# Kernel optimization log

Hardware: AMD Instinct MI355X
Metric: run time of the kernel (lower is better)

## Reference

```python
import jax, jax.numpy as jnp
import numpy as np


def hadamard_matrix(n):
    # Recursive normalized Hadamard matrix of size 2^n (matches the torch code).
    H = np.array([[1.0]])
    for _ in range(n):
        H = np.block([[H, H], [H, -H]]) / np.sqrt(2.0)
    return jnp.asarray(H, dtype=jnp.float32)


def hadamard_conv(x, filt, bias, H):
    # x: (B, Cin, h, w); filt: (F, kh, kw); bias: (F, 1); H: (n, n)
    n = H.shape[0]
    F, kh, kw = filt.shape
    B, C = x.shape[0], x.shape[1]
    # zero-pad filters and data up to (n, n), then 2D Hadamard transform H A H
    kern = jnp.zeros((F, n, n), x.dtype).at[:, :kh, :kw].set(filt)
    kern_t = jnp.matmul(H, jnp.matmul(kern, H))            # (F, n, n)
    data = jnp.zeros((B, C, n, n), x.dtype).at[:, :, : x.shape[2], : x.shape[3]].set(x)
    data_t = jnp.matmul(H, jnp.matmul(data, H))            # (B, C, n, n)
    # Original: expand to (B, C, F, n, n), multiply by kern_t, inverse transform,
    # then sum over C. Since kern_t is independent of C and the transforms are
    # linear, sum over C first -- identical math, no huge intermediate.
    s = data_t.sum(axis=1)                                  # (B, n, n)
    prod = s[:, None, :, :] * kern_t[None, :, :, :]         # (B, F, n, n)
    out = jnp.matmul(H, jnp.matmul(prod, H))                # (B, F, n, n)
    return out + bias[:, 0][None, :, None, None]


def maxpool2(x):
    # 2x2 max pool, stride 2, on (B, C, H, W)
    return jax.lax.reduce_window(x, -jnp.inf, jax.lax.max, (1, 1, 2, 2), (1, 1, 2, 2), 'VALID')


def setup_inputs() -> dict:
    key = jax.random.key(0)
    ks = jax.random.split(key, 9)
    return {
        'x': jax.random.normal(ks[0], (2048, 3, 32, 32), dtype=jnp.float32),
        'filter1': jax.random.normal(ks[1], (32, 3, 3), dtype=jnp.float32),
        'bias1': jax.random.normal(ks[2], (32, 1), dtype=jnp.float32),
        'filter2': jax.random.normal(ks[3], (64, 3, 3), dtype=jnp.float32),
        'bias2': jax.random.normal(ks[4], (64, 1), dtype=jnp.float32),
        'fc1_w': jax.random.normal(ks[5], (512, 4096), dtype=jnp.float32) * 0.02,
        'fc1_b': jax.random.normal(ks[6], (512,), dtype=jnp.float32) * 0.02,
        'fc2_w': jax.random.normal(ks[7], (10, 512), dtype=jnp.float32) * 0.02,
        'fc2_b': jax.random.normal(ks[8], (10,), dtype=jnp.float32) * 0.02,
    }


def reference(x, filter1, bias1, filter2, bias2, fc1_w, fc1_b, fc2_w, fc2_b):
    H1 = hadamard_matrix(5)  # 32x32
    H2 = hadamard_matrix(4)  # 16x16
    out = hadamard_conv(x, filter1, bias1, H1)      # (B, 32, 32, 32)
    out = maxpool2(jax.nn.relu(out))                # (B, 32, 16, 16)
    out = hadamard_conv(out, filter2, bias2, H2)    # (B, 64, 16, 16)
    out = maxpool2(jax.nn.relu(out))                # (B, 64, 8, 8)
    out = out.reshape(-1, 4096)
    out = jax.nn.relu(out @ fc1_w.T + fc1_b)        # (B, 512)
    out = out @ fc2_w.T + fc2_b                     # (B, 10)
    return jax.nn.softmax(out, axis=1)
```

## Files before the change

### kernel.cpp

```cpp
#include <hip/hip_runtime.h>

#define DEVI __device__ __forceinline__

typedef __attribute__((ext_vector_type(8))) short short8x;
typedef __attribute__((ext_vector_type(4))) float float4x;

DEVI float shx(float v, int m) { return __shfl_xor(v, m, 64); }

DEVI unsigned bf16r(float v) {
  unsigned u = __float_as_uint(v);
  return (u + 0x7FFF + ((u >> 16) & 1)) >> 16;
}
DEVI void split2(float a, float b, unsigned& h, unsigned& l) {
  unsigned ra = bf16r(a), rb = bf16r(b);
  float fa = __uint_as_float(ra << 16), fb = __uint_as_float(rb << 16);
  unsigned la = bf16r(a - fa), lb = bf16r(b - fb);
  h = ra | (rb << 16);
  l = la | (lb << 16);
}

DEVI void gload16(const void* g, void* l) {
  __builtin_amdgcn_global_load_lds(
      (const __attribute__((address_space(1))) void*)g,
      (__attribute__((address_space(3))) void*)l, 16, 0, 0);
}

template <int MASK>
DEVI float lanex(float x) {
  if constexpr (MASK == 1)
    return __int_as_float(__builtin_amdgcn_update_dpp(
        0, __float_as_int(x), 0xB1, 0xF, 0xF, true));
  else if constexpr (MASK == 2)
    return __int_as_float(__builtin_amdgcn_update_dpp(
        0, __float_as_int(x), 0x4E, 0xF, 0xF, true));
  else
    return __int_as_float(__builtin_amdgcn_ds_swizzle(
        __float_as_int(x), (MASK << 10) | 0x1F));
}

__global__ __launch_bounds__(256) void k_conv(
    const float* __restrict__ x, const float* __restrict__ filt1,
    const float* __restrict__ bias1, const float* __restrict__ filt2,
    const float* __restrict__ bias2, unsigned short* __restrict__ Ah,
    unsigned short* __restrict__ Al, const float* __restrict__ fc1w,
    unsigned short* __restrict__ Wh, unsigned short* __restrict__ Wl, int B) {
  __shared__ float sP[4 * 320];
  const int b = blockIdx.x;
  const int tid = threadIdx.x;

  if (b >= B) {
    const int wb = b - B;
#pragma unroll
    for (int q = 0; q < 4; ++q) {
      const int i = wb * 4096 + q * 1024 + tid * 4;
      float4 v = *(const float4*)(fc1w + i);
      unsigned h0, l0, h1, l1;
      split2(v.x, v.y, h0, l0);
      split2(v.z, v.w, h1, l1);
      *(uint2*)(Wh + i) = make_uint2(h0, h1);
      *(uint2*)(Wl + i) = make_uint2(l0, l1);
    }
    return;
  }

  const int wv = tid >> 6, t = tid & 63;

  float s0[16];
  {
    const float* xb = x + (size_t)b * 3072 + (t >> 1) * 32 + (t & 1) * 16;
#pragma unroll
    for (int q = 0; q < 4; ++q) {
      float4 a0 = *(const float4*)(xb + 4 * q);
      float4 a1 = *(const float4*)(xb + 1024 + 4 * q);
      float4 a2 = *(const float4*)(xb + 2048 + 4 * q);
      s0[4 * q + 0] = (a0.x + a1.x + a2.x) * (1.0f / 32.0f);
      s0[4 * q + 1] = (a0.y + a1.y + a2.y) * (1.0f / 32.0f);
      s0[4 * q + 2] = (a0.z + a1.z + a2.z) * (1.0f / 32.0f);
      s0[4 * q + 3] = (a0.w + a1.w + a2.w) * (1.0f / 32.0f);
    }
  }
  float s1[16], s2[16];
#pragma unroll
  for (int k = 0; k < 16; ++k) s1[k] = lanex<2>(s0[k]);
#pragma unroll
  for (int k = 0; k < 16; ++k) s2[k] = lanex<4>(s0[k]);

  float acc[8];
#pragma unroll
  for (int j = 0; j < 8; ++j) acc[j] = 0.0f;

  for (int i = 0; i < 8; ++i) {
    const int f = __builtin_amdgcn_readfirstlane(wv * 8 + i);
    const float* fp = filt1 + f * 9;
    float w[9];
#pragma unroll
    for (int k = 0; k < 9; ++k) w[k] = fp[k];
    const float bb = bias1[f];
    float c[8];
#pragma unroll
    for (int p = 0; p < 8; ++p) {
      const int ja = 2 * p, jb = ja ^ 1;
      const int ja2 = ja ^ 2, jb2 = jb ^ 2;
      float va = fmaf(w[0], s0[ja], bb);
      va = fmaf(w[1], s0[jb], va);
      va = fmaf(w[2], s0[ja2], va);
      va = fmaf(w[3], s1[ja], va);
      va = fmaf(w[4], s1[jb], va);
      va = fmaf(w[5], s1[ja2], va);
      va = fmaf(w[6], s2[ja], va);
      va = fmaf(w[7], s2[jb], va);
      va = fmaf(w[8], s2[ja2], va);
      float vb = fmaf(w[0], s0[jb], bb);
      vb = fmaf(w[1], s0[ja], vb);
      vb = fmaf(w[2], s0[jb2], vb);
      vb = fmaf(w[3], s1[jb], vb);
      vb = fmaf(w[4], s1[ja], vb);
      vb = fmaf(w[5], s1[jb2], vb);
      vb = fmaf(w[6], s2[jb], vb);
      vb = fmaf(w[7], s2[ja], vb);
      vb = fmaf(w[8], s2[jb2], vb);
      c[p] = fmaxf(fmaxf(va, vb), 0.0f);
    }
#pragma unroll
    for (int p = 0; p < 8; ++p) acc[p] += fmaxf(c[p], lanex<2>(c[p]));
  }

  if (!(t & 2)) {
    const int pb = wv * 320 + (t >> 2) * 20 + (t & 1) * 8;
    *(float4*)&sP[pb] = make_float4(acc[0], acc[1], acc[2], acc[3]);
    *(float4*)&sP[pb + 4] = make_float4(acc[4], acc[5], acc[6], acc[7]);
  }
  __syncthreads();

  const int f2s = t >> 4, rr = t & 15;
  float r0[16];
#pragma unroll
  for (int q = 0; q < 4; ++q) {
    float4 s = make_float4(0.f, 0.f, 0.f, 0.f);
#pragma unroll
    for (int w2 = 0; w2 < 4; ++w2) {
      const float4 v = *(const float4*)&sP[w2 * 320 + rr * 20 + 4 * q];
      s.x += v.x; s.y += v.y; s.z += v.z; s.w += v.w;
    }
    r0[4 * q + 0] = s.x * (1.0f / 16.0f);
    r0[4 * q + 1] = s.y * (1.0f / 16.0f);
    r0[4 * q + 2] = s.z * (1.0f / 16.0f);
    r0[4 * q + 3] = s.w * (1.0f / 16.0f);
  }
  float r1[16], r2[16];
#pragma unroll
  for (int k = 0; k < 16; ++k) r1[k] = lanex<1>(r0[k]);
#pragma unroll
  for (int k = 0; k < 16; ++k) r2[k] = lanex<2>(r0[k]);

#pragma unroll
  for (int it = 0; it < 4; ++it) {
    const int g = wv * 16 + it * 4 + f2s;
    const float* gp = filt2 + g * 9;
    float w[9];
#pragma unroll
    for (int k = 0; k < 9; ++k) w[k] = gp[k];
    const float bb = bias2[g];
    float c[8];
#pragma unroll
    for (int p = 0; p < 8; ++p) {
      const int ja = 2 * p, jb = ja ^ 1;
      const int ja2 = ja ^ 2, jb2 = jb ^ 2;
      float va = fmaf(w[0], r0[ja], bb);
      va = fmaf(w[1], r0[jb], va);
      va = fmaf(w[2], r0[ja2], va);
      va = fmaf(w[3], r1[ja], va);
      va = fmaf(w[4], r1[jb], va);
      va = fmaf(w[5], r1[ja2], va);
      va = fmaf(w[6], r2[ja], va);
      va = fmaf(w[7], r2[jb], va);
      va = fmaf(w[8], r2[ja2], va);
      float vb = fmaf(w[0], r0[jb], bb);
      vb = fmaf(w[1], r0[ja], vb);
      vb = fmaf(w[2], r0[jb2], vb);
      vb = fmaf(w[3], r1[jb], vb);
      vb = fmaf(w[4], r1[ja], vb);
      vb = fmaf(w[5], r1[jb2], vb);
      vb = fmaf(w[6], r2[jb], vb);
      vb = fmaf(w[7], r2[ja], vb);
      vb = fmaf(w[8], r2[jb2], vb);
      c[p] = fmaxf(fmaxf(va, vb), 0.0f);
    }
#pragma unroll
    for (int p = 0; p < 8; ++p) c[p] = fmaxf(c[p], lanex<1>(c[p]));
    if (!(t & 1)) {
      unsigned hh[4], ll[4];
#pragma unroll
      for (int j = 0; j < 4; ++j) split2(c[2 * j], c[2 * j + 1], hh[j], ll[j]);
      const size_t off = (size_t)b * 4096 + g * 64 + (rr >> 1) * 8;
      *(uint4*)(Ah + off) = make_uint4(hh[0], hh[1], hh[2], hh[3]);
      *(uint4*)(Al + off) = make_uint4(ll[0], ll[1], ll[2], ll[3]);
    }
  }
}

__global__ __launch_bounds__(256) void k_fc1(
    const unsigned short* __restrict__ Ah, const unsigned short* __restrict__ Al,
    const unsigned short* __restrict__ Wh, const unsigned short* __restrict__ Wl,
    float* __restrict__ P, int M) {
  __shared__ __align__(16) unsigned char lds[49152];
  const int bid = blockIdx.x;
  const int c = bid & 127, nt = bid >> 7;
  const int mt = c >> 2, kidx = c & 3;
  const int m0 = mt * 64, n0 = nt * 64, k0 = kidx * 1024;

  const int tid = threadIdx.x;
  const int wv = tid >> 6, lane = tid & 63;
  const int wm = (wv >> 1) * 32, wn = (wv & 1) * 32;
  const int lm = lane & 15, lq = lane >> 4;
  const int rj = lane >> 3, pj = lane & 7;

  float4x acc[2][2];
#pragma unroll
  for (int i = 0; i < 2; ++i)
#pragma unroll
    for (int j = 0; j < 2; ++j) acc[i][j] = (float4x){0.f, 0.f, 0.f, 0.f};

  auto stage = [&](int st, int bb) {
    const int kcol = k0 + st * 32;
#pragma unroll
    for (int it = 0; it < 2; ++it) {
      const int rb = wv * 16 + it * 8;
      const int r = rb + rj;
      const int l = pj ^ (r & 7);
      const unsigned short* src = (l < 4) ? Ah : Al;
      const size_t go = (size_t)(m0 + r) * 4096 + kcol + (l & 3) * 8;
      gload16(src + go, lds + bb + rb * 128);
    }
#pragma unroll
    for (int it = 0; it < 2; ++it) {
      const int rb = wv * 16 + it * 8;
      const int r = rb + rj;
      const int l = pj ^ (r & 7);
      const unsigned short* src = (l < 4) ? Wh : Wl;
      const size_t go = (size_t)(n0 + r) * 4096 + kcol + (l & 3) * 8;
      gload16(src + go, lds + bb + 8192 + rb * 128);
    }
  };

  stage(0, 0);
  stage(1, 16384);
  asm volatile("s_waitcnt vmcnt(4) lgkmcnt(0)" ::: "memory");
  __builtin_amdgcn_sched_barrier(0);
  __builtin_amdgcn_s_barrier();
  __builtin_amdgcn_sched_barrier(0);

  for (int st = 0; st < 32; ++st) {
    const int bb = (st % 3) * 16384;
    if (st < 30) {
      stage(st + 2, ((st + 2) % 3) * 16384);
      __builtin_amdgcn_sched_barrier(0);
    }

    short8x a_h[2], a_l[2], b_h[2], b_l[2];
#pragma unroll
    for (int fm = 0; fm < 2; ++fm) {
      const int r = wm + fm * 16 + lm;
      const unsigned char* base = lds + bb + r * 128;
      a_h[fm] = *(const short8x*)(base + (lq ^ (r & 7)) * 16);
      a_l[fm] = *(const short8x*)(base + ((lq ^ 4) ^ (r & 7)) * 16);
    }
#pragma unroll
    for (int fn = 0; fn < 2; ++fn) {
      const int r = wn + fn * 16 + lm;
      const unsigned char* base = lds + bb + 8192 + r * 128;
      b_h[fn] = *(const short8x*)(base + (lq ^ (r & 7)) * 16);
      b_l[fn] = *(const short8x*)(base + ((lq ^ 4) ^ (r & 7)) * 16);
    }
#pragma unroll
    for (int fm = 0; fm < 2; ++fm)
#pragma unroll
      for (int fn = 0; fn < 2; ++fn) {
        acc[fm][fn] = __builtin_amdgcn_mfma_f32_16x16x32_bf16(
            a_h[fm], b_h[fn], acc[fm][fn], 0, 0, 0);
        acc[fm][fn] = __builtin_amdgcn_mfma_f32_16x16x32_bf16(
            a_h[fm], b_l[fn], acc[fm][fn], 0, 0, 0);
        acc[fm][fn] = __builtin_amdgcn_mfma_f32_16x16x32_bf16(
            a_l[fm], b_h[fn], acc[fm][fn], 0, 0, 0);
      }

    if (st < 31) {
      if (st < 29)
        asm volatile("s_waitcnt vmcnt(4) lgkmcnt(0)" ::: "memory");
      else
        asm volatile("s_waitcnt vmcnt(0) lgkmcnt(0)" ::: "memory");
      __builtin_amdgcn_sched_barrier(0);
      __builtin_amdgcn_s_barrier();
      __builtin_amdgcn_sched_barrier(0);
    }
  }

  float* Pp = P + (size_t)kidx * ((size_t)M * 512);
#pragma unroll
  for (int fm = 0; fm < 2; ++fm)
#pragma unroll
    for (int fn = 0; fn < 2; ++fn)
#pragma unroll
      for (int i = 0; i < 4; ++i) {
        const int r = m0 + wm + fm * 16 + lq * 4 + i;
        const int cc = n0 + wn + fn * 16 + lm;
        Pp[(size_t)r * 512 + cc] = acc[fm][fn][i];
      }
}

__global__ __launch_bounds__(256) void k_fc2(
    const float* __restrict__ P, const float* __restrict__ bias1,
    const float* __restrict__ W, const float* __restrict__ bias2,
    float* __restrict__ out, int M) {
  const int wv = threadIdx.x >> 6, t = threadIdx.x & 63;
  const int b = blockIdx.x * 4 + wv;
  const size_t ks = (size_t)M * 512;
  const float* pr = P + (size_t)b * 512 + t * 8;
  float4 u0 = *(const float4*)pr;
  float4 u1 = *(const float4*)(pr + 4);
#pragma unroll
  for (int k = 1; k < 4; ++k) {
    const float4 v0 = *(const float4*)(pr + k * ks);
    const float4 v1 = *(const float4*)(pr + k * ks + 4);
    u0.x += v0.x; u0.y += v0.y; u0.z += v0.z; u0.w += v0.w;
    u1.x += v1.x; u1.y += v1.y; u1.z += v1.z; u1.w += v1.w;
  }
  const float4 bb0 = *(const float4*)(bias1 + t * 8);
  const float4 bb1 = *(const float4*)(bias1 + t * 8 + 4);
  float a[8];
  a[0] = fmaxf(u0.x + bb0.x, 0.0f);
  a[1] = fmaxf(u0.y + bb0.y, 0.0f);
  a[2] = fmaxf(u0.z + bb0.z, 0.0f);
  a[3] = fmaxf(u0.w + bb0.w, 0.0f);
  a[4] = fmaxf(u1.x + bb1.x, 0.0f);
  a[5] = fmaxf(u1.y + bb1.y, 0.0f);
  a[6] = fmaxf(u1.z + bb1.z, 0.0f);
  a[7] = fmaxf(u1.w + bb1.w, 0.0f);
  float z[10];
#pragma unroll
  for (int o = 0; o < 10; ++o) {
    const float* wr = W + o * 512 + t * 8;
    const float4 w0 = *(const float4*)wr;
    const float4 w1 = *(const float4*)(wr + 4);
    float s = a[0] * w0.x;
    s = fmaf(a[1], w0.y, s);
    s = fmaf(a[2], w0.z, s);
    s = fmaf(a[3], w0.w, s);
    s = fmaf(a[4], w1.x, s);
    s = fmaf(a[5], w1.y, s);
    s = fmaf(a[6], w1.z, s);
    s = fmaf(a[7], w1.w, s);
    z[o] = s;
  }
#pragma unroll
  for (int m = 1; m < 64; m <<= 1) {
#pragma unroll
    for (int o = 0; o < 10; ++o) z[o] += shx(z[o], m);
  }
#pragma unroll
  for (int o = 0; o < 10; ++o) z[o] += bias2[o];
  float mx = z[0];
#pragma unroll
  for (int o = 1; o < 10; ++o) mx = fmaxf(mx, z[o]);
  float e[10];
  float ssum = 0.0f;
#pragma unroll
  for (int o = 0; o < 10; ++o) {
    e[o] = expf(z[o] - mx);
    ssum += e[o];
  }
  const float inv = 1.0f / ssum;
  if (t == 0) {
    float* dst = out + (size_t)b * 10;
#pragma unroll
    for (int o = 0; o < 10; ++o) dst[o] = e[o] * inv;
  }
}

extern "C" void kernel_launch(void* const* d_in, const int* in_sizes, int n_in,
                              void* d_out, int out_size, void* d_ws,
                              size_t ws_size, hipStream_t stream) {
  const float* x = (const float*)d_in[0];
  const float* f1 = (const float*)d_in[1];
  const float* b1 = (const float*)d_in[2];
  const float* f2 = (const float*)d_in[3];
  const float* b2 = (const float*)d_in[4];
  const float* fc1w = (const float*)d_in[5];
  const float* fc1b = (const float*)d_in[6];
  const float* fc2w = (const float*)d_in[7];
  const float* fc2b = (const float*)d_in[8];
  float* out = (float*)d_out;
  const int B = in_sizes[0] / 3072;

  char* w = (char*)d_ws;
  unsigned short* Ah = (unsigned short*)w;
  unsigned short* Al = (unsigned short*)(w + (size_t)B * 8192);
  unsigned short* Wh = (unsigned short*)(w + (size_t)2 * B * 8192);
  unsigned short* Wl = (unsigned short*)(w + (size_t)2 * B * 8192 + 4194304);
  float* P = (float*)(w + (size_t)2 * B * 8192 + 8388608);

  hipLaunchKernelGGL(k_conv, dim3(B + 512), dim3(256), 0, stream, x, f1, b1,
                     f2, b2, Ah, Al, fc1w, Wh, Wl, B);
  hipLaunchKernelGGL(k_fc1, dim3(1024), dim3(256), 0, stream, Ah, Al, Wh, Wl,
                     P, B);
  hipLaunchKernelGGL(k_fc2, dim3(B / 4), dim3(256), 0, stream, P, fc1b, fc2w,
                     fc2b, out, B);
}
```

Baseline: 159.8 us.

## Use single-wave 32x32 fc1 tiles with barrier-free double buffering

The fc1 split-bf16 GEMM moves from 256-thread blocks on 64x64 output tiles with a three-stage LDS ring and block barriers to 64-thread blocks on 32x32 tiles. Each block is one wave, so it double-buffers its own LDS and only needs vmcnt waits, with no s_barrier. The grid grows to four times as many blocks for more parallelism and smaller LDS per block. In exchange, each A and W tile is reused by fewer outputs, so global and L2 traffic rises, and the block-index decode assumes the batch size.

```diff
diff --git a/kernel.cpp b/kernel.cpp
--- a/kernel.cpp
+++ b/kernel.cpp
@@ -199,19 +199,17 @@
   }
 }
 
-__global__ __launch_bounds__(256) void k_fc1(
+__global__ __launch_bounds__(64) void k_fc1(
     const unsigned short* __restrict__ Ah, const unsigned short* __restrict__ Al,
     const unsigned short* __restrict__ Wh, const unsigned short* __restrict__ Wl,
     float* __restrict__ P, int M) {
-  __shared__ __align__(16) unsigned char lds[49152];
+  __shared__ __align__(16) unsigned char lds[16384];
   const int bid = blockIdx.x;
-  const int c = bid & 127, nt = bid >> 7;
+  const int c = bid & 255, nt = bid >> 8;
   const int mt = c >> 2, kidx = c & 3;
-  const int m0 = mt * 64, n0 = nt * 64, k0 = kidx * 1024;
-
-  const int tid = threadIdx.x;
-  const int wv = tid >> 6, lane = tid & 63;
-  const int wm = (wv >> 1) * 32, wn = (wv & 1) * 32;
+  const int m0 = mt * 32, n0 = nt * 32, k0 = kidx * 1024;
+
+  const int lane = threadIdx.x;
   const int lm = lane & 15, lq = lane >> 4;
   const int rj = lane >> 3, pj = lane & 7;
 
@@ -224,8 +222,8 @@
   auto stage = [&](int st, int bb) {
     const int kcol = k0 + st * 32;
 #pragma unroll
-    for (int it = 0; it < 2; ++it) {
-      const int rb = wv * 16 + it * 8;
+    for (int it = 0; it < 4; ++it) {
+      const int rb = it * 8;
       const int r = rb + rj;
       const int l = pj ^ (r & 7);
       const unsigned short* src = (l < 4) ? Ah : Al;
@@ -233,42 +231,40 @@
       gload16(src + go, lds + bb + rb * 128);
     }
 #pragma unroll
-    for (int it = 0; it < 2; ++it) {
-      const int rb = wv * 16 + it * 8;
+    for (int it = 0; it < 4; ++it) {
+      const int rb = it * 8;
       const int r = rb + rj;
       const int l = pj ^ (r & 7);
       const unsigned short* src = (l < 4) ? Wh : Wl;
       const size_t go = (size_t)(n0 + r) * 4096 + kcol + (l & 3) * 8;
-      gload16(src + go, lds + bb + 8192 + rb * 128);
+      gload16(src + go, lds + bb + 4096 + rb * 128);
     }
   };
 
   stage(0, 0);
-  stage(1, 16384);
-  asm volatile("s_waitcnt vmcnt(4) lgkmcnt(0)" ::: "memory");
-  __builtin_amdgcn_sched_barrier(0);
-  __builtin_amdgcn_s_barrier();
-  __builtin_amdgcn_sched_barrier(0);
 
   for (int st = 0; st < 32; ++st) {
-    const int bb = (st % 3) * 16384;
-    if (st < 30) {
-      stage(st + 2, ((st + 2) % 3) * 16384);
-      __builtin_amdgcn_sched_barrier(0);
-    }
+    const int bb = (st & 1) * 8192;
+    if (st < 31) {
+      stage(st + 1, bb ^ 8192);
+      asm volatile("s_waitcnt vmcnt(8)" ::: "memory");
+    } else {
+      asm volatile("s_waitcnt vmcnt(0)" ::: "memory");
+    }
+    __builtin_amdgcn_sched_barrier(0);
 
     short8x a_h[2], a_l[2], b_h[2], b_l[2];
 #pragma unroll
     for (int fm = 0; fm < 2; ++fm) {
-      const int r = wm + fm * 16 + lm;
+      const int r = fm * 16 + lm;
       const unsigned char* base = lds + bb + r * 128;
       a_h[fm] = *(const short8x*)(base + (lq ^ (r & 7)) * 16);
       a_l[fm] = *(const short8x*)(base + ((lq ^ 4) ^ (r & 7)) * 16);
     }
 #pragma unroll
     for (int fn = 0; fn < 2; ++fn) {
-      const int r = wn + fn * 16 + lm;
-      const unsigned char* base = lds + bb + 8192 + r * 128;
+      const int r = fn * 16 + lm;
+      const unsigned char* base = lds + bb + 4096 + r * 128;
       b_h[fn] = *(const short8x*)(base + (lq ^ (r & 7)) * 16);
       b_l[fn] = *(const short8x*)(base + ((lq ^ 4) ^ (r & 7)) * 16);
     }
@@ -283,16 +279,6 @@
         acc[fm][fn] = __builtin_amdgcn_mfma_f32_16x16x32_bf16(
             a_l[fm], b_h[fn], acc[fm][fn], 0, 0, 0);
       }
-
-    if (st < 31) {
-      if (st < 29)
-        asm volatile("s_waitcnt vmcnt(4) lgkmcnt(0)" ::: "memory");
-      else
-        asm volatile("s_waitcnt vmcnt(0) lgkmcnt(0)" ::: "memory");
-      __builtin_amdgcn_sched_barrier(0);
-      __builtin_amdgcn_s_barrier();
-      __builtin_amdgcn_sched_barrier(0);
-    }
   }
 
   float* Pp = P + (size_t)kidx * ((size_t)M * 512);
@@ -302,8 +288,8 @@
     for (int fn = 0; fn < 2; ++fn)
 #pragma unroll
       for (int i = 0; i < 4; ++i) {
-        const int r = m0 + wm + fm * 16 + lq * 4 + i;
-        const int cc = n0 + wn + fn * 16 + lm;
+        const int r = m0 + fm * 16 + lq * 4 + i;
+        const int cc = n0 + fn * 16 + lm;
         Pp[(size_t)r * 512 + cc] = acc[fm][fn][i];
       }
 }
@@ -401,8 +387,8 @@
 
   hipLaunchKernelGGL(k_conv, dim3(B + 512), dim3(256), 0, stream, x, f1, b1,
                      f2, b2, Ah, Al, fc1w, Wh, Wl, B);
-  hipLaunchKernelGGL(k_fc1, dim3(1024), dim3(256), 0, stream, Ah, Al, Wh, Wl,
-                     P, B);
+  hipLaunchKernelGGL(k_fc1, dim3((B / 32) * 4 * (512 / 32)), dim3(64), 0,
+                     stream, Ah, Al, Wh, Wl, P, B);
   hipLaunchKernelGGL(k_fc2, dim3(B / 4), dim3(256), 0, stream, P, fc1b, fc2w,
                      fc2b, out, B);
 }
```

After: 202.3 us. +26.6%, slower.
